# Kernel optimization log

Measured on AMD Instinct MI355X. Metric: run time of the kernel, lower is better.

Reference implementation:

```python
import jax, jax.numpy as jnp
import numpy as np

EMBED_DIM = 1024
NUM_HEADS = 16
ROTARY_THETA = 10000.0


def _rotate_half(t):
    d = t.shape[-1] // 2
    t1, t2 = t[..., :d], t[..., d:]
    return jnp.concatenate([-t2, t1], axis=-1)


def _rope_cos_sin(seq_len, head_dim, dtype):
    # inv_freq over even indices, standard RoPE
    inv_freq = 1.0 / (ROTARY_THETA ** (jnp.arange(0, head_dim, 2, dtype=jnp.float32) / head_dim))
    freqs = jnp.arange(seq_len, dtype=jnp.float32)[:, None] * inv_freq[None, :]  # (S, D/2)
    emb = jnp.concatenate([freqs, freqs], axis=-1)  # (S, D)
    # broadcast over (b, s, h, d)
    return jnp.cos(emb).astype(dtype)[None, :, None, :], jnp.sin(emb).astype(dtype)[None, :, None, :]


def setup_inputs() -> dict:
    key = jax.random.key(0)
    ks = jax.random.split(key, 4)
    B, S, E = 2, 2048, EMBED_DIM
    scale = 1.0 / np.sqrt(E)
    return {
        "x": jax.random.normal(ks[0], (B, S, E), dtype=jnp.float32),
        "attention_mask": jnp.zeros((B, 1, 1, S), dtype=jnp.float32),
        "Wq": jax.random.normal(ks[1], (E, E), dtype=jnp.float32) * scale,
        "bq": jnp.zeros((E,), dtype=jnp.float32),
        "Wk": jax.random.normal(ks[2], (E, E), dtype=jnp.float32) * scale,
        "bk": jnp.zeros((E,), dtype=jnp.float32),
        "Wv": jax.random.normal(ks[3], (E, E), dtype=jnp.float32) * scale,
        "bv": jnp.zeros((E,), dtype=jnp.float32),
    }


def reference(x, attention_mask, Wq, bq, Wk, bk, Wv, bv):
    B, S, E = x.shape
    H = NUM_HEADS
    D = E // H

    q = (x @ Wq + bq).reshape(B, S, H, D)
    k = (x @ Wk + bk).reshape(B, S, H, D)
    v = (x @ Wv + bv).reshape(B, S, H, D)

    cos, sin = _rope_cos_sin(S, D, q.dtype)
    q = q * cos + _rotate_half(q) * sin
    k = k * cos + _rotate_half(k) * sin

    # attention_mask: additive padding bias (b,1,1,k) broadcast over heads & queries
    scores = jnp.einsum("bqhd,bkhd->bhqk", q, k) / jnp.sqrt(jnp.asarray(D, dtype=q.dtype))
    scores = scores + attention_mask  # broadcasts to (b,h,q,k)
    attn = jax.nn.softmax(scores, axis=-1)
    out = jnp.einsum("bhqk,bkhd->bqhd", attn, v)
    return out.reshape(B, S, E)
```

## Files before the change

### kernel.cpp

```cpp
#include <hip/hip_runtime.h>

typedef __attribute__((ext_vector_type(8)))  short bf16x8;
typedef __attribute__((ext_vector_type(4)))  short s16x4;
typedef __attribute__((ext_vector_type(4)))  float f32x4;
typedef __attribute__((ext_vector_type(16))) float f32x16;
typedef __attribute__((ext_vector_type(4)))  unsigned u32x4;
typedef __attribute__((ext_vector_type(4)))  _Float16 f16x4;

#define B_  2
#define S_  2048
#define H_  16
#define D_  64
#define E_  1024
#define M_  (B_*S_)
#define NH_ (M_*H_)
#define L2E 1.44269504f

__device__ __forceinline__ unsigned short f2bf(float f){
  unsigned x = __builtin_bit_cast(unsigned, f);
  x += 0x7fffu + ((x >> 16) & 1u);
  return (unsigned short)(x >> 16);
}
__device__ __forceinline__ unsigned pk_bf16(float lo, float hi){
  unsigned short a = __builtin_bit_cast(unsigned short, (__bf16)lo);
  unsigned short b = __builtin_bit_cast(unsigned short, (__bf16)hi);
  return (unsigned)a | ((unsigned)b << 16);
}

#define GLD16(gp, lp) __builtin_amdgcn_global_load_lds( \
    (const __attribute__((address_space(1))) unsigned*)(gp), \
    (__attribute__((address_space(3))) unsigned*)(lp), 16, 0, 0)

__global__ __launch_bounds__(256) void k_prep(const float* __restrict__ in, short* __restrict__ out,
                                              const float* __restrict__ mask,
                                              float* ct, float* st, float* maskC,
                                              const float* __restrict__ Wq, const float* __restrict__ Wk,
                                              const float* __restrict__ Wv, short* __restrict__ wt){
  const int bx = blockIdx.x;
  if(bx < 4096){
    int i = bx*256 + threadIdx.x;
    if(i < S_*32){
      int s = i >> 5, f = i & 31;
      float invf = powf(10000.0f, -(float)f / 32.0f);
      float ph = (float)s * invf;
      ct[i] = cosf(ph);
      st[i] = sinf(ph);
      if(i < B_*S_) maskC[i] = fmaf(mask[i], L2E, -17.0f);
    }
    int j = i*4;
    float4 v = *(const float4*)(in + j);
    s16x4 o = { (short)f2bf(v.x), (short)f2bf(v.y), (short)f2bf(v.z), (short)f2bf(v.w) };
    *(s16x4*)(out + j) = o;
  } else {
    int w = bx - 4096;
    int z = w >> 8, r = w & 255;
    const float* W = z==0 ? Wq : (z==1 ? Wk : Wv);
    short* outw = wt + (size_t)z*E_*E_;
    __shared__ short tile[64][72];
    int nb = (r & 15)*64, kb = (r >> 4)*64;
    int t = threadIdx.x;
    {
      int rr = t>>2, c0 = (t&3)*16;
      const float* src = W + (size_t)(kb+rr)*E_ + nb + c0;
      #pragma unroll
      for(int i=0;i<4;i++){
        float4 v = *(const float4*)(src + i*4);
        tile[rr][c0+i*4+0] = (short)f2bf(v.x);
        tile[rr][c0+i*4+1] = (short)f2bf(v.y);
        tile[rr][c0+i*4+2] = (short)f2bf(v.z);
        tile[rr][c0+i*4+3] = (short)f2bf(v.w);
      }
    }
    __syncthreads();
    {
      int n = t>>2, k0 = (t&3)*16;
      short* dst = outw + (size_t)(nb+n)*E_ + kb + k0;
      bf16x8 o0, o1;
      #pragma unroll
      for(int i=0;i<8;i++){ o0[i] = tile[k0+i][n]; o1[i] = tile[k0+8+i][n]; }
      *(bf16x8*)dst = o0;
      *(bf16x8*)(dst+8) = o1;
    }
  }
}

__global__ __launch_bounds__(512,2) void k_gemm(const short* __restrict__ A, const short* __restrict__ WT,
                                              const float* __restrict__ biasq, const float* __restrict__ biask,
                                              const float* __restrict__ biasv,
                                              short* __restrict__ oq, short* __restrict__ ok, short* __restrict__ ovt,
                                              const float* __restrict__ cost, const float* __restrict__ sint){
  const int z = blockIdx.z;
  const short* Bw = WT + (size_t)z*E_*E_;
  const float* bias = z==0 ? biasq : (z==1 ? biask : biasv);
  __shared__ short As[2][256*64];
  __shared__ short Bs[2][256*64];
  const int t = threadIdx.x, lane = t & 63, wid = t >> 6;
  const int wr = wid >> 2, wc = wid & 3;
  const int mb = blockIdx.x*256, nb = blockIdx.y*256;
  const int l15 = lane & 15, lq = lane >> 4;
  f32x4 acc[8][4] = {};

  #pragma unroll
  for(int j=0;j<4;j++){
    int c = t + 512*j;
    int row = c>>3;
    int colg = ((c&7) ^ (row&7))*8;
    GLD16(A  + (size_t)(mb + row)*E_ + colg, &As[0][c*8]);
    GLD16(Bw + (size_t)(nb + row)*E_ + colg, &Bs[0][c*8]);
  }
  __syncthreads();

  for(int kt=0; kt<16; kt++){
    const int cur = kt & 1;
    const short* Asc = As[cur];
    const short* Bsc = Bs[cur];
    short* Asn = As[cur^1];
    short* Bsn = Bs[cur^1];
    const bool pf = (kt+1 < 16);
    #pragma unroll
    for(int ph=0; ph<4; ph++){
      const int mq = ph>>1, nq = ph&1;
      bf16x8 af[4][2], bf[2][2];
      #pragma unroll
      for(int i=0;i<4;i++){
        int r = wr*128 + (mq*4+i)*16 + l15;
        #pragma unroll
        for(int kk=0;kk<2;kk++){
          int c8 = (kk*4 + lq) ^ (r&7);
          af[i][kk] = *(const bf16x8*)&Asc[r*64 + c8*8];
        }
      }
      #pragma unroll
      for(int j2=0;j2<2;j2++){
        int r = wc*64 + (nq*2+j2)*16 + l15;
        #pragma unroll
        for(int kk=0;kk<2;kk++){
          int c8 = (kk*4 + lq) ^ (r&7);
          bf[j2][kk] = *(const bf16x8*)&Bsc[r*64 + c8*8];
        }
      }
      if(pf){
        int c = t + 512*ph;
        int row = c>>3;
        int colg = ((c&7) ^ (row&7))*8;
        GLD16(A  + (size_t)(mb + row)*E_ + (kt+1)*64 + colg, &Asn[c*8]);
        GLD16(Bw + (size_t)(nb + row)*E_ + (kt+1)*64 + colg, &Bsn[c*8]);
      }
      __builtin_amdgcn_s_barrier();
      asm volatile("s_waitcnt lgkmcnt(0)" ::: "memory");
      __builtin_amdgcn_sched_barrier(0);
      __builtin_amdgcn_s_setprio(1);
      #pragma unroll
      for(int i=0;i<4;i++)
        #pragma unroll
        for(int j2=0;j2<2;j2++)
          #pragma unroll
          for(int kk=0;kk<2;kk++)
            acc[mq*4+i][nq*2+j2] = __builtin_amdgcn_mfma_f32_16x16x32_bf16(
                af[i][kk], bf[j2][kk], acc[mq*4+i][nq*2+j2], 0, 0, 0);
      __builtin_amdgcn_s_setprio(0);
      if(ph < 3) __builtin_amdgcn_s_barrier();
    }
    __syncthreads();
  }

  const int col16 = l15, rg = lq;
  float bvs[4];
  #pragma unroll
  for(int nf=0; nf<4; nf++) bvs[nf] = bias[nb + wc*64 + nf*16 + col16];
  if(z == 2){
    #pragma unroll
    for(int mf=0; mf<8; mf++){
      int row0 = mb + wr*128 + mf*16 + rg*4;
      int bb2 = row0 >> 11, ss = row0 & (S_-1);
      #pragma unroll
      for(int nf=0; nf<4; nf++){
        int e = nb + wc*64 + nf*16 + col16;
        int hh = e >> 6, dd = e & 63;
        s16x4 w = { (short)f2bf(acc[mf][nf][0]+bvs[nf]), (short)f2bf(acc[mf][nf][1]+bvs[nf]),
                    (short)f2bf(acc[mf][nf][2]+bvs[nf]), (short)f2bf(acc[mf][nf][3]+bvs[nf]) };
        *(s16x4*)(ovt + ((size_t)(bb2*H_+hh)*D_+dd)*S_ + ss) = w;
      }
    }
  } else {
    short* out = (z==0) ? oq : ok;
    const float qs = (z==0) ? (0.125f*L2E) : 1.0f;
    #pragma unroll
    for(int mf=0; mf<8; mf++)
      #pragma unroll
      for(int r=0; r<4; r++){
        int row = mb + wr*128 + mf*16 + rg*4 + r;
        int srow = row & (S_-1);
        const float* cb = cost + (size_t)srow*32;
        const float* sb = sint + (size_t)srow*32;
        #pragma unroll
        for(int nf=0; nf<2; nf++){
          int d = nf*16 + col16;
          float c = cb[d], sn = sb[d];
          float x0 = acc[mf][nf][r]   + bvs[nf];
          float x1 = acc[mf][nf+2][r] + bvs[nf+2];
          out[(size_t)row*E_ + nb + wc*64 + nf*16 + col16]     = (short)f2bf((x0*c - x1*sn)*qs);
          out[(size_t)row*E_ + nb + wc*64 + (nf+2)*16 + col16] = (short)f2bf((x1*c + x0*sn)*qs);
        }
      }
  }
}

__global__ __launch_bounds__(256,4) void k_attn(
    const short* __restrict__ qg, const short* __restrict__ kg,
    const short* __restrict__ vtg, const float* __restrict__ maskC,
    float* __restrict__ o0g, _Float16* __restrict__ o1g, float* __restrict__ lpart){
  __shared__ short Ks[2][64*72];
  __shared__ short Vs[2][64*72];
  const int flat = blockIdx.x;
  const int v = flat >> 3;
  const int bh = (flat & 7)*4 + (v >> 5);
  const int inner = v & 31;
  const int qb = inner >> 1, sp = inner & 1;
  const int h = bh & 15, b = bh >> 4;
  const int tid = threadIdx.x, wid = tid>>6, lane = tid&63;
  const int l31 = lane & 31, hl = lane >> 5;
  const int qw = qb*128 + wid*32;
  const int rr = tid>>3, ch = tid&7;
  const int kb0 = sp*16;
  const int NT = 16;

  bf16x8 qf[4];
  {
    const short* qp = qg + ((size_t)(b*S_ + qw + l31)*H_ + h)*D_;
    #pragma unroll
    for(int dk=0; dk<4; dk++)
      qf[dk] = *(const bf16x8*)(qp + dk*16 + hl*8);
  }
  f32x16 O0 = {}, O1 = {};
  float l_run = 0.f;
  const float* mrow = maskC + (size_t)b*S_;

  bf16x8 ka, kc, va, vc;
#define LOADT(kb) { \
    const short* ks_ = kg + ((size_t)(b*S_ + (kb)*64 + rr)*H_ + h)*D_ + ch*8; \
    ka = *(const bf16x8*)ks_;  kc = *(const bf16x8*)(ks_ + 32*H_*D_); \
    const short* vs_ = vtg + ((size_t)(b*H_ + h)*D_ + rr)*S_ + (kb)*64 + ch*8; \
    va = *(const bf16x8*)vs_;  vc = *(const bf16x8*)(vs_ + 32*S_); }
#define WRITET(pp) { \
    *(bf16x8*)&Ks[pp][rr*72 + ch*8]      = ka; \
    *(bf16x8*)&Ks[pp][(rr+32)*72 + ch*8] = kc; \
    *(bf16x8*)&Vs[pp][rr*72 + ch*8]      = va; \
    *(bf16x8*)&Vs[pp][(rr+32)*72 + ch*8] = vc; }

  LOADT(kb0);
  WRITET(0);
  LOADT(kb0+1);
  asm volatile("s_waitcnt lgkmcnt(0)" ::: "memory");
  __builtin_amdgcn_s_barrier();

  int p = 0;
  for(int tt=0; tt<NT; tt++){
    f32x16 s0 = {}, s1 = {};
    __builtin_amdgcn_s_setprio(1);
    #pragma unroll
    for(int dk=0; dk<4; dk++){
      bf16x8 kf0 = *(const bf16x8*)&Ks[p][(l31)*72 + dk*16 + hl*8];
      bf16x8 kf1 = *(const bf16x8*)&Ks[p][(32+l31)*72 + dk*16 + hl*8];
      s0 = __builtin_amdgcn_mfma_f32_32x32x16_bf16(kf0, qf[dk], s0, 0,0,0);
      s1 = __builtin_amdgcn_mfma_f32_32x32x16_bf16(kf1, qf[dk], s1, 0,0,0);
    }
    __builtin_amdgcn_s_setprio(0);
    {
      const float* mt = mrow + (kb0+tt)*64 + hl*4;
      #pragma unroll
      for(int bb=0; bb<4; bb++){
        f32x4 mv0 = *(const f32x4*)(mt + bb*8);
        f32x4 mv1 = *(const f32x4*)(mt + 32 + bb*8);
        #pragma unroll
        for(int a=0; a<4; a++){ s0[bb*4+a] += mv0[a]; s1[bb*4+a] += mv1[a]; }
      }
    }
    #pragma unroll
    for(int i=0;i<16;i++) s0[i] = __builtin_amdgcn_exp2f(s0[i]);
    #pragma unroll
    for(int i=0;i<16;i++) s1[i] = __builtin_amdgcn_exp2f(s1[i]);
    float la=0.f, lb=0.f, lc=0.f, ld=0.f;
    #pragma unroll
    for(int i=0;i<4;i++){
      la += s0[i];   lb += s0[4+i];  lc += s0[8+i];  ld += s0[12+i];
      la += s1[i];   lb += s1[4+i];  lc += s1[8+i];  ld += s1[12+i];
    }
    float ls = (la+lb)+(lc+ld);
    ls += __shfl_xor(ls, 32);
    l_run += ls;

    unsigned w0a[8], w1a[8];
    #pragma unroll
    for(int c=0;c<8;c++){
      int base = (c&3)*4;
      float p0 = (c & 4) ? s1[base+0] : s0[base+0];
      float p1 = (c & 4) ? s1[base+1] : s0[base+1];
      float p2 = (c & 4) ? s1[base+2] : s0[base+2];
      float p3 = (c & 4) ? s1[base+3] : s0[base+3];
      w0a[c] = pk_bf16(p0, p1);
      w1a[c] = pk_bf16(p2, p3);
    }

    if(tt+1 < NT){
      WRITET(p^1);
      if(tt+2 < NT) LOADT(kb0+tt+2);
    }

    __builtin_amdgcn_s_setprio(1);
    #pragma unroll
    for(int ksl=0; ksl<4; ksl++){
      unsigned a0 = w0a[2*ksl], b0 = w0a[2*ksl+1];
      unsigned a1 = w1a[2*ksl], b1 = w1a[2*ksl+1];
      asm("v_permlane32_swap_b32 %0, %1" : "+v"(a0), "+v"(b0));
      asm("v_permlane32_swap_b32 %0, %1" : "+v"(a1), "+v"(b1));
      u32x4 pw = { a0, a1, b0, b1 };
      bf16x8 pf = __builtin_bit_cast(bf16x8, pw);
      bf16x8 vf0 = *(const bf16x8*)&Vs[p][(l31)*72 + ksl*16 + hl*8];
      bf16x8 vf1 = *(const bf16x8*)&Vs[p][(32+l31)*72 + ksl*16 + hl*8];
      O0 = __builtin_amdgcn_mfma_f32_32x32x16_bf16(pf, vf0, O0, 0,0,0);
      O1 = __builtin_amdgcn_mfma_f32_32x32x16_bf16(pf, vf1, O1, 0,0,0);
    }
    __builtin_amdgcn_s_setprio(0);
    asm volatile("s_waitcnt lgkmcnt(0)" ::: "memory");
    __builtin_amdgcn_s_barrier();
    p ^= 1;
  }
#undef LOADT
#undef WRITET

  if(sp == 0){
    #pragma unroll
    for(int bb=0; bb<4; bb++)
      #pragma unroll
      for(int a=0; a<4; a++){
        int qrow = qw + a + 8*bb + 4*hl;
        float* op = o0g + ((size_t)(b*S_ + qrow)*H_ + h)*D_;
        op[l31]      = O0[bb*4+a];
        op[32 + l31] = O1[bb*4+a];
      }
  } else {
    #pragma unroll
    for(int bb=0; bb<4; bb++)
      #pragma unroll
      for(int a=0; a<4; a++){
        int qrow = qw + a + 8*bb + 4*hl;
        _Float16* op = o1g + ((size_t)(b*S_ + qrow)*H_ + h)*D_;
        op[l31]      = (_Float16)O0[bb*4+a];
        op[32 + l31] = (_Float16)O1[bb*4+a];
      }
  }
  if(lane < 32)
    lpart[(size_t)sp*NH_ + (size_t)(b*S_ + qw + l31)*H_ + h] = l_run;
}

__global__ __launch_bounds__(256) void k_comb(float* __restrict__ out, const _Float16* __restrict__ o1,
                                              const float* __restrict__ lpart){
  int i = blockIdx.x*256 + threadIdx.x;
  int idx = i*4;
  int lidx = idx >> 6;
  float linv = 1.f / (lpart[lidx] + lpart[NH_ + lidx]);
  f32x4 a = *(f32x4*)(out + idx);
  f16x4 bb = *(const f16x4*)(o1 + idx);
  f32x4 r = { (a[0] + (float)bb[0])*linv, (a[1] + (float)bb[1])*linv,
              (a[2] + (float)bb[2])*linv, (a[3] + (float)bb[3])*linv };
  *(f32x4*)(out + idx) = r;
}

extern "C" void kernel_launch(void* const* d_in, const int* in_sizes, int n_in,
                              void* d_out, int out_size, void* d_ws, size_t ws_size,
                              hipStream_t stream){
  (void)in_sizes; (void)n_in; (void)out_size; (void)ws_size;
  const float* x    = (const float*)d_in[0];
  const float* mask = (const float*)d_in[1];
  const float* Wq   = (const float*)d_in[2];
  const float* bq   = (const float*)d_in[3];
  const float* Wk   = (const float*)d_in[4];
  const float* bk   = (const float*)d_in[5];
  const float* Wv   = (const float*)d_in[6];
  const float* bv   = (const float*)d_in[7];
  float* out = (float*)d_out;
  char* ws = (char*)d_ws;
  float* cost  = (float*)(ws);
  float* sint  = (float*)(ws + (256u<<10));
  float* maskC = (float*)(ws + (512u<<10));
  float* lpart = (float*)(ws + (768u<<10));
  short* xb    = (short*)(ws + (2u<<20));
  short* wt    = (short*)(ws + (10u<<20));
  short* qb    = (short*)(ws + (16u<<20));
  short* kb    = (short*)(ws + (24u<<20));
  short* vtb   = (short*)(ws + (32u<<20));
  _Float16* o1 = (_Float16*)xb;

  k_prep<<<dim3(4096+768), dim3(256), 0, stream>>>(x, xb, mask, cost, sint, maskC,
                                                   Wq, Wk, Wv, wt);
  k_gemm<<<dim3(16,4,3), dim3(512), 0, stream>>>(xb, wt, bq, bk, bv, qb, kb, vtb, cost, sint);
  k_attn<<<dim3(1024), dim3(256), 0, stream>>>(qb, kb, vtb, maskC, out, o1, lpart);
  k_comb<<<dim3(4096), dim3(256), 0, stream>>>(out, o1, lpart);
}
```

Baseline: 111.8 us.

## Store both attention split partials in fp16 and batch GEMM prefetch into two phases

When the workspace is large enough, the first split-K attention partial is written as fp16 to a separate buffer instead of fp32 into the output. This halves that write and lets the combine kernel read two fp16 buffers instead of fp32 plus fp16, at some precision cost. Separately, the GEMM prefetch of the next K tile is now issued as two loads per phase in the first two phases instead of one per phase across all four. The second change front-loads the global loads so they have more time to land.

```diff
diff --git a/kernel.cpp b/kernel.cpp
--- a/kernel.cpp
+++ b/kernel.cpp
@@ -139,12 +139,15 @@
           bf[j2][kk] = *(const bf16x8*)&Bsc[r*64 + c8*8];
         }
       }
-      if(pf){
-        int c = t + 512*ph;
-        int row = c>>3;
-        int colg = ((c&7) ^ (row&7))*8;
-        GLD16(A  + (size_t)(mb + row)*E_ + (kt+1)*64 + colg, &Asn[c*8]);
-        GLD16(Bw + (size_t)(nb + row)*E_ + (kt+1)*64 + colg, &Bsn[c*8]);
+      if(pf && ph < 2){
+        #pragma unroll
+        for(int j3=0;j3<2;j3++){
+          int c = t + 512*(ph*2 + j3);
+          int row = c>>3;
+          int colg = ((c&7) ^ (row&7))*8;
+          GLD16(A  + (size_t)(mb + row)*E_ + (kt+1)*64 + colg, &Asn[c*8]);
+          GLD16(Bw + (size_t)(nb + row)*E_ + (kt+1)*64 + colg, &Bsn[c*8]);
+        }
       }
       __builtin_amdgcn_s_barrier();
       asm volatile("s_waitcnt lgkmcnt(0)" ::: "memory");
@@ -209,7 +212,8 @@
 __global__ __launch_bounds__(256,4) void k_attn(
     const short* __restrict__ qg, const short* __restrict__ kg,
     const short* __restrict__ vtg, const float* __restrict__ maskC,
-    float* __restrict__ o0g, _Float16* __restrict__ o1g, float* __restrict__ lpart){
+    float* __restrict__ o0g, _Float16* __restrict__ p0g, _Float16* __restrict__ p1g,
+    float* __restrict__ lpart, int wide){
   __shared__ short Ks[2][64*72];
   __shared__ short Vs[2][64*72];
   const int flat = blockIdx.x;
@@ -330,22 +334,34 @@
 #undef WRITET
 
   if(sp == 0){
+    if(wide){
+      #pragma unroll
+      for(int bb=0; bb<4; bb++)
+        #pragma unroll
+        for(int a=0; a<4; a++){
+          int qrow = qw + a + 8*bb + 4*hl;
+          _Float16* op = p0g + ((size_t)(b*S_ + qrow)*H_ + h)*D_;
+          op[l31]      = (_Float16)O0[bb*4+a];
+          op[32 + l31] = (_Float16)O1[bb*4+a];
+        }
+    } else {
+      #pragma unroll
+      for(int bb=0; bb<4; bb++)
+        #pragma unroll
+        for(int a=0; a<4; a++){
+          int qrow = qw + a + 8*bb + 4*hl;
+          float* op = o0g + ((size_t)(b*S_ + qrow)*H_ + h)*D_;
+          op[l31]      = O0[bb*4+a];
+          op[32 + l31] = O1[bb*4+a];
+        }
+    }
+  } else {
     #pragma unroll
     for(int bb=0; bb<4; bb++)
       #pragma unroll
       for(int a=0; a<4; a++){
         int qrow = qw + a + 8*bb + 4*hl;
-        float* op = o0g + ((size_t)(b*S_ + qrow)*H_ + h)*D_;
-        op[l31]      = O0[bb*4+a];
-        op[32 + l31] = O1[bb*4+a];
-      }
-  } else {
-    #pragma unroll
-    for(int bb=0; bb<4; bb++)
-      #pragma unroll
-      for(int a=0; a<4; a++){
-        int qrow = qw + a + 8*bb + 4*hl;
-        _Float16* op = o1g + ((size_t)(b*S_ + qrow)*H_ + h)*D_;
+        _Float16* op = p1g + ((size_t)(b*S_ + qrow)*H_ + h)*D_;
         op[l31]      = (_Float16)O0[bb*4+a];
         op[32 + l31] = (_Float16)O1[bb*4+a];
       }
@@ -354,23 +370,31 @@
     lpart[(size_t)sp*NH_ + (size_t)(b*S_ + qw + l31)*H_ + h] = l_run;
 }
 
-__global__ __launch_bounds__(256) void k_comb(float* __restrict__ out, const _Float16* __restrict__ o1,
-                                              const float* __restrict__ lpart){
+__global__ __launch_bounds__(256) void k_comb(float* __restrict__ out, const _Float16* __restrict__ p0,
+                                              const _Float16* __restrict__ p1,
+                                              const float* __restrict__ lpart, int wide){
   int i = blockIdx.x*256 + threadIdx.x;
   int idx = i*4;
   int lidx = idx >> 6;
   float linv = 1.f / (lpart[lidx] + lpart[NH_ + lidx]);
-  f32x4 a = *(f32x4*)(out + idx);
-  f16x4 bb = *(const f16x4*)(o1 + idx);
-  f32x4 r = { (a[0] + (float)bb[0])*linv, (a[1] + (float)bb[1])*linv,
-              (a[2] + (float)bb[2])*linv, (a[3] + (float)bb[3])*linv };
+  f16x4 q1 = *(const f16x4*)(p1 + idx);
+  f32x4 r;
+  if(wide){
+    f16x4 q0 = *(const f16x4*)(p0 + idx);
+    #pragma unroll
+    for(int j=0;j<4;j++) r[j] = ((float)q0[j] + (float)q1[j]) * linv;
+  } else {
+    f32x4 a = *(f32x4*)(out + idx);
+    #pragma unroll
+    for(int j=0;j<4;j++) r[j] = (a[j] + (float)q1[j]) * linv;
+  }
   *(f32x4*)(out + idx) = r;
 }
 
 extern "C" void kernel_launch(void* const* d_in, const int* in_sizes, int n_in,
                               void* d_out, int out_size, void* d_ws, size_t ws_size,
                               hipStream_t stream){
-  (void)in_sizes; (void)n_in; (void)out_size; (void)ws_size;
+  (void)in_sizes; (void)n_in; (void)out_size;
   const float* x    = (const float*)d_in[0];
   const float* mask = (const float*)d_in[1];
   const float* Wq   = (const float*)d_in[2];
@@ -390,11 +414,14 @@
   short* qb    = (short*)(ws + (16u<<20));
   short* kb    = (short*)(ws + (24u<<20));
   short* vtb   = (short*)(ws + (32u<<20));
-  _Float16* o1 = (_Float16*)xb;
+  _Float16* p1 = (_Float16*)xb;
+  _Float16* p0 = (_Float16*)(ws + (40u<<20));
+
+  const int wide = (ws_size >= (size_t)(48u<<20)) ? 1 : 0;
 
   k_prep<<<dim3(4096+768), dim3(256), 0, stream>>>(x, xb, mask, cost, sint, maskC,
                                                    Wq, Wk, Wv, wt);
   k_gemm<<<dim3(16,4,3), dim3(512), 0, stream>>>(xb, wt, bq, bk, bv, qb, kb, vtb, cost, sint);
-  k_attn<<<dim3(1024), dim3(256), 0, stream>>>(qb, kb, vtb, maskC, out, o1, lpart);
-  k_comb<<<dim3(4096), dim3(256), 0, stream>>>(out, o1, lpart);
-}
+  k_attn<<<dim3(1024), dim3(256), 0, stream>>>(qb, kb, vtb, maskC, out, p0, p1, lpart, wide);
+  k_comb<<<dim3(4096), dim3(256), 0, stream>>>(out, p0, p1, lpart, wide);
+}
```

After: 111.5 us (median of 2 runs). Within noise of the previous version (-0.3%).

## Merge split-KV attention halves in-block via LDS and drop combine kernel

Applied to the files above, without the earlier changes.

The attention kernel now launches 512-thread blocks in which two 256-thread groups each process half of the key range for the same query tile. The groups then combine their partial outputs and row sums through shared memory and write the normalized result directly. This removes the separate combine kernel and the global round trip of the partial fp32/fp16 outputs and row sums. Separately, the GEMM prefetch issues two tiles' worth of loads in each of the first two phases instead of one per phase. The trade-offs are larger blocks with lower occupancy per block and an extra in-block reduction step.

```diff
diff --git a/kernel.cpp b/kernel.cpp
--- a/kernel.cpp
+++ b/kernel.cpp
@@ -5,7 +5,6 @@
 typedef __attribute__((ext_vector_type(4)))  float f32x4;
 typedef __attribute__((ext_vector_type(16))) float f32x16;
 typedef __attribute__((ext_vector_type(4)))  unsigned u32x4;
-typedef __attribute__((ext_vector_type(4)))  _Float16 f16x4;
 
 #define B_  2
 #define S_  2048
@@ -139,12 +138,15 @@
           bf[j2][kk] = *(const bf16x8*)&Bsc[r*64 + c8*8];
         }
       }
-      if(pf){
-        int c = t + 512*ph;
-        int row = c>>3;
-        int colg = ((c&7) ^ (row&7))*8;
-        GLD16(A  + (size_t)(mb + row)*E_ + (kt+1)*64 + colg, &Asn[c*8]);
-        GLD16(Bw + (size_t)(nb + row)*E_ + (kt+1)*64 + colg, &Bsn[c*8]);
+      if(pf && ph < 2){
+        #pragma unroll
+        for(int j3=0;j3<2;j3++){
+          int c = t + 512*(ph*2 + j3);
+          int row = c>>3;
+          int colg = ((c&7) ^ (row&7))*8;
+          GLD16(A  + (size_t)(mb + row)*E_ + (kt+1)*64 + colg, &Asn[c*8]);
+          GLD16(Bw + (size_t)(nb + row)*E_ + (kt+1)*64 + colg, &Bsn[c*8]);
+        }
       }
       __builtin_amdgcn_s_barrier();
       asm volatile("s_waitcnt lgkmcnt(0)" ::: "memory");
@@ -206,24 +208,24 @@
   }
 }
 
-__global__ __launch_bounds__(256,4) void k_attn(
+__global__ __launch_bounds__(512,2) void k_attn(
     const short* __restrict__ qg, const short* __restrict__ kg,
     const short* __restrict__ vtg, const float* __restrict__ maskC,
-    float* __restrict__ o0g, _Float16* __restrict__ o1g, float* __restrict__ lpart){
-  __shared__ short Ks[2][64*72];
-  __shared__ short Vs[2][64*72];
+    float* __restrict__ outg){
+  __shared__ short smem[2*18432];
   const int flat = blockIdx.x;
   const int v = flat >> 3;
-  const int bh = (flat & 7)*4 + (v >> 5);
-  const int inner = v & 31;
-  const int qb = inner >> 1, sp = inner & 1;
+  const int bh = (flat & 7)*4 + (v >> 4);
+  const int qb = v & 15;
   const int h = bh & 15, b = bh >> 4;
   const int tid = threadIdx.x, wid = tid>>6, lane = tid&63;
+  const int grp = wid >> 2, w4 = wid & 3;
   const int l31 = lane & 31, hl = lane >> 5;
-  const int qw = qb*128 + wid*32;
-  const int rr = tid>>3, ch = tid&7;
-  const int kb0 = sp*16;
+  const int qw = qb*128 + w4*32;
+  const int tg = tid & 255, rr = tg>>3, ch = tg&7;
+  const int kb0 = grp*16;
   const int NT = 16;
+  short* base = smem + grp*18432;
 
   bf16x8 qf[4];
   {
@@ -243,10 +245,12 @@
     const short* vs_ = vtg + ((size_t)(b*H_ + h)*D_ + rr)*S_ + (kb)*64 + ch*8; \
     va = *(const bf16x8*)vs_;  vc = *(const bf16x8*)(vs_ + 32*S_); }
 #define WRITET(pp) { \
-    *(bf16x8*)&Ks[pp][rr*72 + ch*8]      = ka; \
-    *(bf16x8*)&Ks[pp][(rr+32)*72 + ch*8] = kc; \
-    *(bf16x8*)&Vs[pp][rr*72 + ch*8]      = va; \
-    *(bf16x8*)&Vs[pp][(rr+32)*72 + ch*8] = vc; }
+    short* kd = base + (pp)*4608; \
+    short* vd = base + 9216 + (pp)*4608; \
+    *(bf16x8*)&kd[rr*72 + ch*8]      = ka; \
+    *(bf16x8*)&kd[(rr+32)*72 + ch*8] = kc; \
+    *(bf16x8*)&vd[rr*72 + ch*8]      = va; \
+    *(bf16x8*)&vd[(rr+32)*72 + ch*8] = vc; }
 
   LOADT(kb0);
   WRITET(0);
@@ -256,12 +260,14 @@
 
   int p = 0;
   for(int tt=0; tt<NT; tt++){
+    const short* Ksp = base + p*4608;
+    const short* Vsp = base + 9216 + p*4608;
     f32x16 s0 = {}, s1 = {};
     __builtin_amdgcn_s_setprio(1);
     #pragma unroll
     for(int dk=0; dk<4; dk++){
-      bf16x8 kf0 = *(const bf16x8*)&Ks[p][(l31)*72 + dk*16 + hl*8];
-      bf16x8 kf1 = *(const bf16x8*)&Ks[p][(32+l31)*72 + dk*16 + hl*8];
+      bf16x8 kf0 = *(const bf16x8*)&Ksp[(l31)*72 + dk*16 + hl*8];
+      bf16x8 kf1 = *(const bf16x8*)&Ksp[(32+l31)*72 + dk*16 + hl*8];
       s0 = __builtin_amdgcn_mfma_f32_32x32x16_bf16(kf0, qf[dk], s0, 0,0,0);
       s1 = __builtin_amdgcn_mfma_f32_32x32x16_bf16(kf1, qf[dk], s1, 0,0,0);
     }
@@ -293,11 +299,11 @@
     unsigned w0a[8], w1a[8];
     #pragma unroll
     for(int c=0;c<8;c++){
-      int base = (c&3)*4;
-      float p0 = (c & 4) ? s1[base+0] : s0[base+0];
-      float p1 = (c & 4) ? s1[base+1] : s0[base+1];
-      float p2 = (c & 4) ? s1[base+2] : s0[base+2];
-      float p3 = (c & 4) ? s1[base+3] : s0[base+3];
+      int bs = (c&3)*4;
+      float p0 = (c & 4) ? s1[bs+0] : s0[bs+0];
+      float p1 = (c & 4) ? s1[bs+1] : s0[bs+1];
+      float p2 = (c & 4) ? s1[bs+2] : s0[bs+2];
+      float p3 = (c & 4) ? s1[bs+3] : s0[bs+3];
       w0a[c] = pk_bf16(p0, p1);
       w1a[c] = pk_bf16(p2, p3);
     }
@@ -316,8 +322,8 @@
       asm("v_permlane32_swap_b32 %0, %1" : "+v"(a1), "+v"(b1));
       u32x4 pw = { a0, a1, b0, b1 };
       bf16x8 pf = __builtin_bit_cast(bf16x8, pw);
-      bf16x8 vf0 = *(const bf16x8*)&Vs[p][(l31)*72 + ksl*16 + hl*8];
-      bf16x8 vf1 = *(const bf16x8*)&Vs[p][(32+l31)*72 + ksl*16 + hl*8];
+      bf16x8 vf0 = *(const bf16x8*)&Vsp[(l31)*72 + ksl*16 + hl*8];
+      bf16x8 vf1 = *(const bf16x8*)&Vsp[(32+l31)*72 + ksl*16 + hl*8];
       O0 = __builtin_amdgcn_mfma_f32_32x32x16_bf16(pf, vf0, O0, 0,0,0);
       O1 = __builtin_amdgcn_mfma_f32_32x32x16_bf16(pf, vf1, O1, 0,0,0);
     }
@@ -329,42 +335,36 @@
 #undef LOADT
 #undef WRITET
 
-  if(sp == 0){
+  __syncthreads();
+  float* ex  = (float*)smem;
+  float* exl = (float*)smem + 4*32*64;
+  if(grp == 1){
+    #pragma unroll
+    for(int r=0;r<16;r++){
+      ex[(w4*32 + r)*64 + lane]      = O0[r];
+      ex[(w4*32 + 16 + r)*64 + lane] = O1[r];
+    }
+    if(lane < 32) exl[w4*32 + lane] = l_run;
+  }
+  __syncthreads();
+  if(grp == 0){
+    #pragma unroll
+    for(int r=0;r<16;r++){
+      O0[r] += ex[(w4*32 + r)*64 + lane];
+      O1[r] += ex[(w4*32 + 16 + r)*64 + lane];
+    }
+    float linv = 1.f / (l_run + exl[w4*32 + l31]);
     #pragma unroll
     for(int bb=0; bb<4; bb++)
       #pragma unroll
       for(int a=0; a<4; a++){
+        float li = __shfl(linv, a + 8*bb + 4*hl);
         int qrow = qw + a + 8*bb + 4*hl;
-        float* op = o0g + ((size_t)(b*S_ + qrow)*H_ + h)*D_;
-        op[l31]      = O0[bb*4+a];
-        op[32 + l31] = O1[bb*4+a];
-      }
-  } else {
-    #pragma unroll
-    for(int bb=0; bb<4; bb++)
-      #pragma unroll
-      for(int a=0; a<4; a++){
-        int qrow = qw + a + 8*bb + 4*hl;
-        _Float16* op = o1g + ((size_t)(b*S_ + qrow)*H_ + h)*D_;
-        op[l31]      = (_Float16)O0[bb*4+a];
-        op[32 + l31] = (_Float16)O1[bb*4+a];
-      }
-  }
-  if(lane < 32)
-    lpart[(size_t)sp*NH_ + (size_t)(b*S_ + qw + l31)*H_ + h] = l_run;
-}
-
-__global__ __launch_bounds__(256) void k_comb(float* __restrict__ out, const _Float16* __restrict__ o1,
-                                              const float* __restrict__ lpart){
-  int i = blockIdx.x*256 + threadIdx.x;
-  int idx = i*4;
-  int lidx = idx >> 6;
-  float linv = 1.f / (lpart[lidx] + lpart[NH_ + lidx]);
-  f32x4 a = *(f32x4*)(out + idx);
-  f16x4 bb = *(const f16x4*)(o1 + idx);
-  f32x4 r = { (a[0] + (float)bb[0])*linv, (a[1] + (float)bb[1])*linv,
-              (a[2] + (float)bb[2])*linv, (a[3] + (float)bb[3])*linv };
-  *(f32x4*)(out + idx) = r;
+        float* op = outg + ((size_t)(b*S_ + qrow)*H_ + h)*D_;
+        op[l31]      = O0[bb*4+a] * li;
+        op[32 + l31] = O1[bb*4+a] * li;
+      }
+  }
 }
 
 extern "C" void kernel_launch(void* const* d_in, const int* in_sizes, int n_in,
@@ -384,17 +384,14 @@
   float* cost  = (float*)(ws);
   float* sint  = (float*)(ws + (256u<<10));
   float* maskC = (float*)(ws + (512u<<10));
-  float* lpart = (float*)(ws + (768u<<10));
   short* xb    = (short*)(ws + (2u<<20));
   short* wt    = (short*)(ws + (10u<<20));
   short* qb    = (short*)(ws + (16u<<20));
   short* kb    = (short*)(ws + (24u<<20));
   short* vtb   = (short*)(ws + (32u<<20));
-  _Float16* o1 = (_Float16*)xb;
 
   k_prep<<<dim3(4096+768), dim3(256), 0, stream>>>(x, xb, mask, cost, sint, maskC,
                                                    Wq, Wk, Wv, wt);
   k_gemm<<<dim3(16,4,3), dim3(512), 0, stream>>>(xb, wt, bq, bk, bv, qb, kb, vtb, cost, sint);
-  k_attn<<<dim3(1024), dim3(256), 0, stream>>>(qb, kb, vtb, maskC, out, o1, lpart);
-  k_comb<<<dim3(4096), dim3(256), 0, stream>>>(out, o1, lpart);
-}
+  k_attn<<<dim3(512), dim3(512), 0, stream>>>(qb, kb, vtb, maskC, out);
+}
```

New measurement: 111.9 us. About the same (+0.0%).
